# Kernel tuning notes

Measured on AMD Instinct MI355X. Metric: run time of the kernel, lower is better.

## Reference

```python
import jax, jax.numpy as jnp
import numpy as np
from jax import lax

B, C, H, W = 8, 1024, 64, 48
A = 9  # anchors per location

def _conv(x, w, b, pad):
    y = lax.conv_general_dilated(x, w, (1, 1), pad,
                                 dimension_numbers=('NCHW', 'OIHW', 'NCHW'))
    return y + b[None, :, None, None]

def setup_inputs() -> dict:
    key = jax.random.key(0)
    ks = jax.random.split(key, 12)
    base_feat = jax.random.normal(ks[0], (B, C, H, W), dtype=jnp.float32)
    W_conv = jax.random.normal(ks[1], (512, C, 3, 3), dtype=jnp.float32) * 0.01
    b_conv = jnp.zeros((512,), jnp.float32)
    W_cls = jax.random.normal(ks[2], (18, 512, 1, 1), dtype=jnp.float32) * 0.01
    b_cls = jnp.zeros((18,), jnp.float32)
    W_bbox = jax.random.normal(ks[3], (36, 512, 1, 1), dtype=jnp.float32) * 0.01
    b_bbox = jnp.zeros((36,), jnp.float32)
    # anchor-target-layer outputs (data-dependent assignment) provided as inputs
    rpn_label = (jax.random.randint(ks[4], (B, A * H * W), 0, 3) - 1).astype(jnp.int32)  # {-1,0,1}
    rpn_bbox_targets = jax.random.normal(ks[5], (B, 36, H, W), dtype=jnp.float32) * 0.1
    rpn_bbox_inside_weights = (jax.random.uniform(ks[6], (B, 36, H, W)) < 0.25).astype(jnp.float32)
    rpn_bbox_outside_weights = jax.random.uniform(ks[7], (B, 36, H, W), dtype=jnp.float32) * 0.01
    return {"base_feat": base_feat, "W_conv": W_conv, "b_conv": b_conv,
            "W_cls": W_cls, "b_cls": b_cls, "W_bbox": W_bbox, "b_bbox": b_bbox,
            "rpn_label": rpn_label, "rpn_bbox_targets": rpn_bbox_targets,
            "rpn_bbox_inside_weights": rpn_bbox_inside_weights,
            "rpn_bbox_outside_weights": rpn_bbox_outside_weights}

def reference(base_feat, W_conv, b_conv, W_cls, b_cls, W_bbox, b_bbox,
              rpn_label, rpn_bbox_targets, rpn_bbox_inside_weights,
              rpn_bbox_outside_weights):
    # RPN head: 3x3 conv + relu, then 1x1 cls / bbox heads
    rpn_conv1 = jax.nn.relu(_conv(base_feat, W_conv, b_conv, ((1, 1), (1, 1))))
    cls_score = _conv(rpn_conv1, W_cls, b_cls, ((0, 0), (0, 0)))   # [B,18,H,W]
    bbox_pred = _conv(rpn_conv1, W_bbox, b_bbox, ((0, 0), (0, 0)))  # [B,36,H,W]
    # reshape to [B,2,A*H,W], softmax over the 2-way fg/bg axis, reshape back
    score_rs = cls_score.reshape(B, 2, A * H, W)
    prob_rs = jax.nn.softmax(score_rs, axis=1)
    rpn_cls_prob = prob_rs.reshape(B, 18, H, W)
    # classification loss: permute(0,2,3,1).view(-1,2), keep labels != -1
    logits = score_rs.transpose(0, 2, 3, 1).reshape(-1, 2)
    label = rpn_label.reshape(-1)
    valid = (label != -1).astype(logits.dtype)
    logp = jax.nn.log_softmax(logits, axis=-1)
    lbl = jnp.clip(label, 0, 1)
    nll = -jnp.take_along_axis(logp, lbl[:, None].astype(jnp.int32), axis=1)[:, 0]
    rpn_loss_cls = jnp.sum(nll * valid) / jnp.maximum(jnp.sum(valid), 1.0)
    # smooth-L1 box loss, sigma=3, summed over dims [1,2,3], mean over batch
    sigma2 = 9.0
    in_diff = rpn_bbox_inside_weights * (bbox_pred - rpn_bbox_targets)
    abs_d = jnp.abs(in_diff)
    sign = lax.stop_gradient((abs_d < 1.0 / sigma2).astype(abs_d.dtype))
    in_loss = in_diff * in_diff * (sigma2 / 2.0) * sign + (abs_d - 0.5 / sigma2) * (1.0 - sign)
    rpn_loss_box = jnp.mean(jnp.sum(rpn_bbox_outside_weights * in_loss, axis=(1, 2, 3)))
    return rpn_cls_prob, bbox_pred, rpn_loss_cls, rpn_loss_box
```

## Files before the change

kernel.cpp:

```cpp
#include <hip/hip_runtime.h>
#include <stdint.h>

#define B_    8
#define CIN   1024
#define H_    64
#define W_    48
#define OC    512
#define HW    3072
#define NPOS  24576
#define K9    9216
#define HP    66
#define WP    50

typedef __attribute__((ext_vector_type(8))) __bf16 bf16x8;
typedef __attribute__((ext_vector_type(4))) float  float4_t;
typedef __attribute__((ext_vector_type(4))) unsigned short ushort4_t;
typedef __attribute__((ext_vector_type(8))) int int8v;
typedef __attribute__((ext_vector_type(4))) int int4v;

__device__ __forceinline__ unsigned short f2bf(float x) {
  union { float f; unsigned u; } v; v.f = x;
  unsigned r = v.u + 0x7FFFu + ((v.u >> 16) & 1u);
  return (unsigned short)(r >> 16);
}

__device__ __forceinline__ unsigned int pack4_fp8(float a, float b, float c, float d) {
  int w = __builtin_amdgcn_cvt_pk_fp8_f32(a, b, 0, false);
  w = __builtin_amdgcn_cvt_pk_fp8_f32(c, d, w, true);
  return (unsigned int)w;
}

__device__ __forceinline__ void async16(const void* g, void* l) {
  __builtin_amdgcn_global_load_lds(
      (const __attribute__((address_space(1))) unsigned int*)g,
      (__attribute__((address_space(3))) unsigned int*)l, 16, 0, 0);
}

__device__ __forceinline__ float wave_sum(float v) {
  for (int o = 32; o > 0; o >>= 1) v += __shfl_down(v, o, 64);
  return v;
}

__global__ void prep_fused(const float* __restrict__ x, const float* __restrict__ Wc,
                           const float* __restrict__ Wcls, const float* __restrict__ Wbb,
                           unsigned char* __restrict__ xt, unsigned char* __restrict__ Wa,
                           unsigned short* __restrict__ Wh, float* __restrict__ accbuf) {
  __shared__ float smem[9216];
  int bid = blockIdx.x, t = threadIdx.x;
  if (bid < 4096) {
    int cx = bid & 7, h = (bid >> 3) & 63, b = bid >> 9;
    float* tile = smem;
    const float* src = x + ((long)(b * CIN + cx * 128) * H_ + h) * W_;
    for (int it = 0; it < 6; ++it) {
      int e = it * 256 + t;
      int cl = e / 12, w4 = e % 12;
      float4_t v = *(const float4_t*)&src[(long)cl * HW + w4 * 4];
      int base = cl * 49 + w4 * 4;
      tile[base] = v.x; tile[base + 1] = v.y; tile[base + 2] = v.z; tile[base + 3] = v.w;
    }
    __syncthreads();
    unsigned char* dst = xt + ((long)(b * HP + h + 1) * WP + 1) * CIN + cx * 128;
    for (int it = 0; it < 6; ++it) {
      int e = it * 256 + t;
      int w = e >> 5, g = e & 31;
      float v0 = tile[(g * 4 + 0) * 49 + w] * 16.f;
      float v1 = tile[(g * 4 + 1) * 49 + w] * 16.f;
      float v2 = tile[(g * 4 + 2) * 49 + w] * 16.f;
      float v3 = tile[(g * 4 + 3) * 49 + w] * 16.f;
      *(unsigned int*)&dst[(long)w * CIN + g * 4] = pack4_fp8(v0, v1, v2, v3);
    }
  } else if (bid < 4608) {
    int o = bid - 4096;
    float* lw = smem;
    const float* src = Wc + (long)o * K9;
    for (int i = 0; i < 9; ++i)
      *(float4_t*)&lw[i * 1024 + t * 4] = *(const float4_t*)&src[i * 1024 + t * 4];
    __syncthreads();
    unsigned char* dst = Wa + (long)o * K9;
    int c = t * 4;
    for (int off = 0; off < 9; ++off) {
      float v0 = lw[(c + 0) * 9 + off] * 512.f;
      float v1 = lw[(c + 1) * 9 + off] * 512.f;
      float v2 = lw[(c + 2) * 9 + off] * 512.f;
      float v3 = lw[(c + 3) * 9 + off] * 512.f;
      *(unsigned int*)&dst[off * 1024 + c] = pack4_fp8(v0, v1, v2, v3);
    }
  } else if (bid < 4640) {
    int e = (bid - 4608) * 1024 + t * 4;
    int m = e >> 9, c = e & 511;
    float v0 = 0.f, v1 = 0.f, v2 = 0.f, v3 = 0.f;
    if (m < 18) {
      const float* s = Wcls + m * 512 + c;
      v0 = s[0]; v1 = s[1]; v2 = s[2]; v3 = s[3];
    } else if (m < 54) {
      const float* s = Wbb + (m - 18) * 512 + c;
      v0 = s[0]; v1 = s[1]; v2 = s[2]; v3 = s[3];
    }
    ushort4_t pk; pk.x = f2bf(v0); pk.y = f2bf(v1); pk.z = f2bf(v2); pk.w = f2bf(v3);
    *(ushort4_t*)&Wh[e] = pk;
    if (bid == 4608 && t < 4) accbuf[t] = 0.f;
  } else {
    int bid2 = bid - 4640;
    int b = bid2 / 66, h = bid2 % 66;
    unsigned char* base = xt + (long)(b * 66 + h) * 50 * 1024;
    int4v z = {};
    if (h == 0 || h == 65) {
      for (int i = t; i < 3200; i += 256) *(int4v*)(base + (long)i * 16) = z;
    } else if (t < 128) {
      int which = t >> 6, off = t & 63;
      *(int4v*)(base + (long)which * 49 * 1024 + (long)off * 16) = z;
    }
  }
}

__global__ __launch_bounds__(256, 2)
void conv_gemm(const unsigned char* __restrict__ Wa, const unsigned char* __restrict__ xt,
               const float* __restrict__ bias, unsigned short* __restrict__ conv1) {
  __shared__ unsigned char As_[2][128 * 128];
  __shared__ unsigned char Bt[2560 * 16];
  int t = threadIdx.x;
  int lane = t & 63, wv = t >> 6;
  int m0 = blockIdx.y * 128;
  int n0 = blockIdx.x * 192;
  int wm = wv >> 1, wn = wv & 1;
  int quad = lane >> 4, col = lane & 15;
  int bB = n0 / HW;
  int h0 = (n0 % HW) / W_;

  long bOff[10];
  for (int i = 0; i < 10; ++i) {
    int c = i * 256 + t;
    int p = c >> 3, s = c & 7;
    int pc = (p < 300) ? p : 0;
    int q = s ^ (pc & 7);
    int r = pc / 50, w = pc % 50;
    bOff[i] = ((long)(bB * HP + h0 + r) * WP + w) * CIN + q * 16;
  }
  auto stageB = [&](int cc) {
    long co = (long)cc * 128;
    for (int i = 0; i < 10; ++i)
      async16(xt + bOff[i] + co, &Bt[(i * 256 + wv * 64) * 16]);
  };

  const unsigned char* aSrc[4];
  for (int s = 0; s < 4; ++s) {
    int c = s * 256 + t;
    int r = c >> 3;
    int q = (c & 7) ^ (r & 7);
    aSrc[s] = Wa + (long)(m0 + r) * K9 + q * 16;
  }
  auto stageA = [&](int buf, int aoff) {
    for (int s = 0; s < 4; ++s)
      async16(aSrc[s] + aoff, &As_[buf][s * 4096 + wv * 1024]);
  };

  int pbase[6];
  for (int j = 0; j < 6; ++j) {
    int nl = wn * 96 + j * 16 + col;
    int hl = nl / W_, wl = nl % W_;
    pbase[j] = hl * 50 + wl;
  }

  float4_t acc[4][6] = {};
  int q2 = quad * 2;

  stageB(0);
  stageA(0, 0);
  int abuf = 0;

#pragma unroll 1
  for (int cc = 0; cc < 8; ++cc) {
#pragma unroll 1
    for (int tap = 0; tap < 9; ++tap) {
      asm volatile("s_waitcnt vmcnt(0)\n\ts_barrier" ::: "memory");
      const unsigned char* A = As_[abuf];
      int dy = tap / 3, dx = tap - dy * 3;
      int doff = dy * 50 + dx;
      int8v af[4], bfr[6];
      for (int i = 0; i < 4; ++i) {
        int r = wm * 64 + i * 16 + col;
        int rb = r * 128, x7 = r & 7;
        int4v lo = *(const int4v*)&A[rb + (((q2 + 0) ^ x7) << 4)];
        int4v hi = *(const int4v*)&A[rb + (((q2 + 1) ^ x7) << 4)];
        af[i] = (int8v){lo.x, lo.y, lo.z, lo.w, hi.x, hi.y, hi.z, hi.w};
      }
      for (int j = 0; j < 6; ++j) {
        int pj = pbase[j] + doff;
        int rb = pj << 7, x7 = pj & 7;
        int4v lo = *(const int4v*)&Bt[rb + (((q2 + 0) ^ x7) << 4)];
        int4v hi = *(const int4v*)&Bt[rb + (((q2 + 1) ^ x7) << 4)];
        bfr[j] = (int8v){lo.x, lo.y, lo.z, lo.w, hi.x, hi.y, hi.z, hi.w};
      }
      asm volatile("s_waitcnt lgkmcnt(0)\n\ts_barrier" ::: "memory");
      __builtin_amdgcn_sched_barrier(0);
      int nt = tap + 1, ncc = cc;
      if (nt == 9) { nt = 0; ++ncc; }
      if (ncc < 8) {
        stageA(abuf ^ 1, nt * 1024 + ncc * 128);
        if (nt == 0) stageB(ncc);
      }
      __builtin_amdgcn_sched_barrier(0);
      __builtin_amdgcn_s_setprio(1);
      for (int i = 0; i < 4; ++i)
        for (int j = 0; j < 6; ++j)
          acc[i][j] = __builtin_amdgcn_mfma_scale_f32_16x16x128_f8f6f4(
              af[i], bfr[j], acc[i][j], 0, 0, 0, 0x76767676, 0, 0x7B7B7B7B);
      __builtin_amdgcn_s_setprio(0);
      __builtin_amdgcn_sched_barrier(0);
      abuf ^= 1;
    }
  }

  for (int i = 0; i < 4; ++i) {
    int mb = m0 + wm * 64 + i * 16 + quad * 4;
    float b0 = bias[mb + 0], b1 = bias[mb + 1], b2 = bias[mb + 2], b3 = bias[mb + 3];
    for (int j = 0; j < 6; ++j) {
      int n = n0 + wn * 96 + j * 16 + col;
      ushort4_t pk;
      pk.x = f2bf(fmaxf(acc[i][j].x + b0, 0.f));
      pk.y = f2bf(fmaxf(acc[i][j].y + b1, 0.f));
      pk.z = f2bf(fmaxf(acc[i][j].z + b2, 0.f));
      pk.w = f2bf(fmaxf(acc[i][j].w + b3, 0.f));
      *(ushort4_t*)&conv1[(long)n * 512 + mb] = pk;
    }
  }
}

__global__ __launch_bounds__(256, 2)
void head_gemm(const unsigned short* __restrict__ Wh, const unsigned short* __restrict__ conv1,
               const float* __restrict__ b_cls, const float* __restrict__ b_bbox,
               float* __restrict__ cls_ws, float* __restrict__ out_bbox) {
  __shared__ unsigned short As[64 * 128];
  __shared__ unsigned short Bs[64 * 128];
  int t = threadIdx.x;
  int lane = t & 63, wv = t >> 6;
  int n0 = blockIdx.x * 64;
  int quad = lane >> 4, col = lane & 15;
  const unsigned short* aS[4];
  const unsigned short* bS[4];
  for (int p = 0; p < 4; ++p) {
    int c = p * 256 + t;
    int r = c >> 4;
    int q = (c & 15) ^ (r & 15);
    aS[p] = Wh + (long)r * 512 + q * 8;
    bS[p] = conv1 + (long)(n0 + r) * 512 + q * 8;
  }
  float4_t acc[4] = {};
  for (int kt = 0; kt < 4; ++kt) {
    long koff = (long)kt * 128;
    __syncthreads();
    for (int p = 0; p < 4; ++p) async16(aS[p] + koff, &As[p * 2048 + wv * 512]);
    for (int p = 0; p < 4; ++p) async16(bS[p] + koff, &Bs[p * 2048 + wv * 512]);
    __syncthreads();
    for (int ks = 0; ks < 4; ++ks) {
      int rn = wv * 16 + col;
      bf16x8 bfr = *(const bf16x8*)&Bs[rn * 128 + (((ks * 4 + quad) ^ (rn & 15)) << 3)];
      for (int i = 0; i < 4; ++i) {
        int r = i * 16 + col;
        bf16x8 af = *(const bf16x8*)&As[r * 128 + (((ks * 4 + quad) ^ (r & 15)) << 3)];
        acc[i] = __builtin_amdgcn_mfma_f32_16x16x32_bf16(af, bfr, acc[i], 0, 0, 0);
      }
    }
  }
  int n = n0 + wv * 16 + col;
  int b = n / HW; int rem = n % HW;
  for (int i = 0; i < 4; ++i) {
    for (int r = 0; r < 4; ++r) {
      int m = i * 16 + quad * 4 + r;
      float v = acc[i][r];
      if (m < 18) {
        cls_ws[(long)(b * 18 + m) * HW + rem] = v + b_cls[m];
      } else if (m < 54) {
        out_bbox[(long)(b * 36 + (m - 18)) * HW + rem] = v + b_bbox[m - 18];
      }
    }
  }
}

__global__ void loss_fused(const float* __restrict__ cls, const int* __restrict__ label,
                           float* __restrict__ prob,
                           const float* __restrict__ pred, const float* __restrict__ tgt,
                           const float* __restrict__ iw, const float* __restrict__ ow,
                           float* __restrict__ acc) {
  int lane = threadIdx.x & 63, wv = threadIdx.x >> 6;
  __shared__ float red[8];
  if (blockIdx.x < 864) {
    int idx = blockIdx.x * 256 + threadIdx.x;
    int b = idx / 27648; int r = idx % 27648;
    int a = r / HW; int r2 = r % HW;
    long i0 = (long)(b * 18 + a) * HW + r2;
    long i1 = i0 + (long)9 * HW;
    float x0 = cls[i0], x1 = cls[i1];
    float mx = fmaxf(x0, x1);
    float e0 = __expf(x0 - mx), e1 = __expf(x1 - mx);
    float s = e0 + e1;
    prob[i0] = e0 / s;
    prob[i1] = e1 / s;
    int lb = label[idx];
    float nll = 0.f, val = 0.f;
    if (lb != -1) {
      val = 1.f;
      float xl = (lb > 0) ? x1 : x0;
      nll = -(xl - mx - __logf(s));
    }
    nll = wave_sum(nll);
    val = wave_sum(val);
    if (lane == 0) { red[wv] = nll; red[4 + wv] = val; }
    __syncthreads();
    if (threadIdx.x == 0) {
      atomicAdd(&acc[0], red[0] + red[1] + red[2] + red[3]);
      atomicAdd(&acc[1], red[4] + red[5] + red[6] + red[7]);
    }
  } else {
    int bid = blockIdx.x - 864;
    float s = 0.f;
    const long total = (long)B_ * 36 * HW;
    for (long i = (long)bid * 256 + threadIdx.x; i < total; i += (long)1728 * 256) {
      float d = iw[i] * (pred[i] - tgt[i]);
      float ad = fabsf(d);
      float l = (ad < (1.f / 9.f)) ? d * d * 4.5f : ad - (1.f / 18.f);
      s += ow[i] * l;
    }
    s = wave_sum(s);
    if (lane == 0) red[wv] = s;
    __syncthreads();
    if (threadIdx.x == 0) atomicAdd(&acc[2], red[0] + red[1] + red[2] + red[3]);
  }
}

__global__ void finalize(const float* __restrict__ acc, float* __restrict__ out) {
  if (threadIdx.x == 0) {
    out[0] = acc[0] / fmaxf(acc[1], 1.f);
    out[1] = acc[2] / (float)B_;
  }
}

extern "C" void kernel_launch(void* const* d_in, const int* in_sizes, int n_in,
                              void* d_out, int out_size, void* d_ws, size_t ws_size,
                              hipStream_t stream) {
  const float* base_feat = (const float*)d_in[0];
  const float* W_conv    = (const float*)d_in[1];
  const float* b_conv    = (const float*)d_in[2];
  const float* W_cls     = (const float*)d_in[3];
  const float* b_cls     = (const float*)d_in[4];
  const float* W_bbox    = (const float*)d_in[5];
  const float* b_bbox    = (const float*)d_in[6];
  const int*   rpn_label = (const int*)d_in[7];
  const float* bb_tgt    = (const float*)d_in[8];
  const float* bb_iw     = (const float*)d_in[9];
  const float* bb_ow     = (const float*)d_in[10];

  float* out = (float*)d_out;
  float* out_cls_prob = out;
  float* out_bbox     = out + 442368;
  float* out_scalars  = out + 442368 + 884736;

  size_t off = 0;
  auto alloc = [&](size_t bytes) {
    void* p = (char*)d_ws + off;
    off = (off + bytes + 255) & ~(size_t)255;
    return p;
  };
  const size_t XT_BYTES = (size_t)B_ * HP * WP * CIN;
  unsigned char*  xt    = (unsigned char*)alloc(XT_BYTES);
  unsigned char*  Wa    = (unsigned char*)alloc((size_t)OC * K9);
  unsigned short* conv1 = (unsigned short*)alloc((size_t)NPOS * OC * 2);
  unsigned short* Wh    = (unsigned short*)alloc((size_t)64 * 512 * 2);
  float* cls_ws         = (float*)alloc((size_t)B_ * 18 * HW * 4);
  float* accbuf         = (float*)alloc(16);

  prep_fused<<<5168, 256, 0, stream>>>(base_feat, W_conv, W_cls, W_bbox, xt, Wa, Wh, accbuf);
  conv_gemm<<<dim3(128, 4), 256, 0, stream>>>(Wa, xt, b_conv, conv1);
  head_gemm<<<384, 256, 0, stream>>>(Wh, conv1, b_cls, b_bbox, cls_ws, out_bbox);
  loss_fused<<<2592, 256, 0, stream>>>(cls_ws, rpn_label, out_cls_prob,
                                       out_bbox, bb_tgt, bb_iw, bb_ow, accbuf);
  finalize<<<1, 64, 0, stream>>>(accbuf, out_scalars);
}
```

Baseline: 333.2 us.

## Fuse softmax, cls loss and box loss into head GEMM epilogue

```diff
diff --git a/kernel.cpp b/kernel.cpp
--- a/kernel.cpp
+++ b/kernel.cpp
@@ -229,9 +229,14 @@
 __global__ __launch_bounds__(256, 2)
 void head_gemm(const unsigned short* __restrict__ Wh, const unsigned short* __restrict__ conv1,
                const float* __restrict__ b_cls, const float* __restrict__ b_bbox,
-               float* __restrict__ cls_ws, float* __restrict__ out_bbox) {
+               const int* __restrict__ label, const float* __restrict__ tgt,
+               const float* __restrict__ iw, const float* __restrict__ ow,
+               float* __restrict__ prob, float* __restrict__ out_bbox,
+               float* __restrict__ accbuf) {
   __shared__ unsigned short As[64 * 128];
   __shared__ unsigned short Bs[64 * 128];
+  __shared__ float sacc[64][57];
+  __shared__ float red[12];
   int t = threadIdx.x;
   int lane = t & 63, wv = t >> 6;
   int n0 = blockIdx.x * 64;
@@ -262,69 +267,53 @@
       }
     }
   }
-  int n = n0 + wv * 16 + col;
-  int b = n / HW; int rem = n % HW;
+  int nn_own = wv * 16 + col;
   for (int i = 0; i < 4; ++i) {
     for (int r = 0; r < 4; ++r) {
       int m = i * 16 + quad * 4 + r;
-      float v = acc[i][r];
-      if (m < 18) {
-        cls_ws[(long)(b * 18 + m) * HW + rem] = v + b_cls[m];
-      } else if (m < 54) {
-        out_bbox[(long)(b * 36 + (m - 18)) * HW + rem] = v + b_bbox[m - 18];
-      }
-    }
-  }
-}
-
-__global__ void loss_fused(const float* __restrict__ cls, const int* __restrict__ label,
-                           float* __restrict__ prob,
-                           const float* __restrict__ pred, const float* __restrict__ tgt,
-                           const float* __restrict__ iw, const float* __restrict__ ow,
-                           float* __restrict__ acc) {
-  int lane = threadIdx.x & 63, wv = threadIdx.x >> 6;
-  __shared__ float red[8];
-  if (blockIdx.x < 864) {
-    int idx = blockIdx.x * 256 + threadIdx.x;
-    int b = idx / 27648; int r = idx % 27648;
-    int a = r / HW; int r2 = r % HW;
-    long i0 = (long)(b * 18 + a) * HW + r2;
-    long i1 = i0 + (long)9 * HW;
-    float x0 = cls[i0], x1 = cls[i1];
+      if (m < 54) {
+        float bv = (m < 18) ? b_cls[m] : b_bbox[m - 18];
+        sacc[nn_own][m] = acc[i][r] + bv;
+      }
+    }
+  }
+  __syncthreads();
+
+  int b = n0 / HW; int rem0 = n0 % HW;
+  float nll = 0.f, val = 0.f, box = 0.f;
+  for (int p = t; p < 576; p += 256) {
+    int a = p >> 6, nn = p & 63;
+    float x0 = sacc[nn][a], x1 = sacc[nn][a + 9];
     float mx = fmaxf(x0, x1);
     float e0 = __expf(x0 - mx), e1 = __expf(x1 - mx);
     float s = e0 + e1;
+    long i0 = (long)(b * 18 + a) * HW + rem0 + nn;
     prob[i0] = e0 / s;
-    prob[i1] = e1 / s;
-    int lb = label[idx];
-    float nll = 0.f, val = 0.f;
+    prob[i0 + (long)9 * HW] = e1 / s;
+    int lb = label[b * 27648 + a * HW + rem0 + nn];
     if (lb != -1) {
-      val = 1.f;
+      val += 1.f;
       float xl = (lb > 0) ? x1 : x0;
-      nll = -(xl - mx - __logf(s));
-    }
-    nll = wave_sum(nll);
-    val = wave_sum(val);
-    if (lane == 0) { red[wv] = nll; red[4 + wv] = val; }
-    __syncthreads();
-    if (threadIdx.x == 0) {
-      atomicAdd(&acc[0], red[0] + red[1] + red[2] + red[3]);
-      atomicAdd(&acc[1], red[4] + red[5] + red[6] + red[7]);
-    }
-  } else {
-    int bid = blockIdx.x - 864;
-    float s = 0.f;
-    const long total = (long)B_ * 36 * HW;
-    for (long i = (long)bid * 256 + threadIdx.x; i < total; i += (long)1728 * 256) {
-      float d = iw[i] * (pred[i] - tgt[i]);
-      float ad = fabsf(d);
-      float l = (ad < (1.f / 9.f)) ? d * d * 4.5f : ad - (1.f / 18.f);
-      s += ow[i] * l;
-    }
-    s = wave_sum(s);
-    if (lane == 0) red[wv] = s;
-    __syncthreads();
-    if (threadIdx.x == 0) atomicAdd(&acc[2], red[0] + red[1] + red[2] + red[3]);
+      nll -= (xl - mx - __logf(s));
+    }
+  }
+  for (int e = t; e < 2304; e += 256) {
+    int mb = e >> 6, nn = e & 63;
+    float v = sacc[nn][18 + mb];
+    long g = (long)(b * 36 + mb) * HW + rem0 + nn;
+    out_bbox[g] = v;
+    float d = iw[g] * (v - tgt[g]);
+    float ad = fabsf(d);
+    float l = (ad < (1.f / 9.f)) ? d * d * 4.5f : ad - (1.f / 18.f);
+    box += ow[g] * l;
+  }
+  nll = wave_sum(nll); val = wave_sum(val); box = wave_sum(box);
+  if (lane == 0) { red[wv] = nll; red[4 + wv] = val; red[8 + wv] = box; }
+  __syncthreads();
+  if (t == 0) {
+    atomicAdd(&accbuf[0], red[0] + red[1] + red[2] + red[3]);
+    atomicAdd(&accbuf[1], red[4] + red[5] + red[6] + red[7]);
+    atomicAdd(&accbuf[2], red[8] + red[9] + red[10] + red[11]);
   }
 }
 
@@ -366,13 +355,12 @@
   unsigned char*  Wa    = (unsigned char*)alloc((size_t)OC * K9);
   unsigned short* conv1 = (unsigned short*)alloc((size_t)NPOS * OC * 2);
   unsigned short* Wh    = (unsigned short*)alloc((size_t)64 * 512 * 2);
-  float* cls_ws         = (float*)alloc((size_t)B_ * 18 * HW * 4);
   float* accbuf         = (float*)alloc(16);
 
   prep_fused<<<5168, 256, 0, stream>>>(base_feat, W_conv, W_cls, W_bbox, xt, Wa, Wh, accbuf);
   conv_gemm<<<dim3(128, 4), 256, 0, stream>>>(Wa, xt, b_conv, conv1);
-  head_gemm<<<384, 256, 0, stream>>>(Wh, conv1, b_cls, b_bbox, cls_ws, out_bbox);
-  loss_fused<<<2592, 256, 0, stream>>>(cls_ws, rpn_label, out_cls_prob,
-                                       out_bbox, bb_tgt, bb_iw, bb_ow, accbuf);
+  head_gemm<<<384, 256, 0, stream>>>(Wh, conv1, b_cls, b_bbox,
+                                     rpn_label, bb_tgt, bb_iw, bb_ow,
+                                     out_cls_prob, out_bbox, accbuf);
   finalize<<<1, 64, 0, stream>>>(accbuf, out_scalars);
 }
```

Measured after the change: 304.6 us. 1.09x faster.
